# Kernel optimization log

Hardware: AMD Instinct MI355X
Metric: run time of the kernel (lower is better)

## Reference

```python
import jax, jax.numpy as jnp
import numpy as np

EPS = 1e-05

def setup_inputs() -> dict:
    key = jax.random.key(0)
    inputs = jax.random.normal(key, (32, 512, 768), dtype=jnp.float32)
    return {"inputs": inputs}

def reference(inputs) -> jnp.ndarray:
    # position weight: L2 norm per token, w[b,l] = sqrt(1e-5 + sum_d x^2)
    w = jnp.sqrt(EPS + jnp.sum(inputs * inputs, axis=-1))  # [B, L]
    # output[b,d,e] = sum_l w[b,l] * x[b,l,d] * x[b,l,e]
    # fused weighted Gram matrix; never materializes [B,L,D,D]
    return jnp.einsum('bld,ble->bde', inputs * w[..., None], inputs)
```

## Files before the change

kernel.cpp:

```cpp
#include <hip/hip_runtime.h>
#include <hip/hip_bf16.h>

#define BATCH 32
#define LL 512
#define DD 768
#define EPSC 1e-5f

typedef __attribute__((ext_vector_type(8))) short bf16x8;
typedef __attribute__((ext_vector_type(4))) float f32x4;

__global__ __launch_bounds__(256) void k_prep(const float* __restrict__ x,
                                              ushort* __restrict__ yt) {
    __shared__ float tile[64][65];
    __shared__ float svec[64];
    int lb = blockIdx.x;
    int b = blockIdx.y;
    int l0 = lb * 64;
    int t = threadIdx.x;

    {
        int r = t >> 2, q = t & 3;
        const float4* xr = (const float4*)(x + ((size_t)b * LL + l0 + r) * DD) + q * 48;
        float sum = 0.f;
#pragma unroll 8
        for (int i = 0; i < 48; i++) {
            float4 v = xr[i];
            sum += v.x * v.x + v.y * v.y + v.z * v.z + v.w * v.w;
        }
        sum += __shfl_xor(sum, 1, 64);
        sum += __shfl_xor(sum, 2, 64);
        if (q == 0) svec[r] = sqrtf(sqrtf(EPSC + sum));
    }
    __syncthreads();

    const float* xb = x + ((size_t)b * LL + l0) * DD;
    int f = t & 15, lr0 = t >> 4;
    int lc = t & 7, dl0 = t >> 3;
    for (int dt = 0; dt < 12; dt++) {
        int d0 = dt * 64;
#pragma unroll
        for (int r = 0; r < 4; r++) {
            int l = lr0 + r * 16;
            float4 v = *(const float4*)(xb + (size_t)l * DD + d0 + f * 4);
#pragma unroll
            for (int j = 0; j < 4; j++)
                tile[l][f * 4 + j] = ((const float*)&v)[j];
        }
        __syncthreads();
        ushort* yp = yt + ((size_t)b * DD + d0) * LL + l0;
#pragma unroll
        for (int it = 0; it < 2; it++) {
            int d = dl0 + it * 32;
            bf16x8 w;
#pragma unroll
            for (int j = 0; j < 8; j++) {
                int l = lc * 8 + j;
                float v = tile[l][d] * svec[l];
                __hip_bfloat16 h = __float2bfloat16(v);
                w[j] = *(short*)&h;
            }
            *(bf16x8*)(yp + (size_t)d * LL + lc * 8) = w;
        }
        __syncthreads();
    }
}

__global__ __launch_bounds__(256) void k_gemm(const ushort* __restrict__ yt,
                                              float* __restrict__ out) {
    __shared__ ushort At[2][128 * 64];
    __shared__ ushort Bt[2][128 * 64];
    int i = blockIdx.x;
    int xcd = i & 7, slot = i >> 3;
    int b = xcd + 8 * (slot / 21);
    int p = slot % 21;
    int t = p, tm = 0, rem = 6;
    while (t >= rem) { t -= rem; rem--; tm++; }
    int tn = tm + t;
    bool diag = (tm == tn);
    int m0 = tm * 128, n0 = tn * 128;
    int tid = threadIdx.x;
    int wave = tid >> 6, lane = tid & 63;
    int wr = wave >> 1, wc = wave & 1;
    const ushort* yb = yt + (size_t)b * DD * LL;

    f32x4 acc[4][4];
#pragma unroll
    for (int ii = 0; ii < 4; ii++)
#pragma unroll
        for (int j = 0; j < 4; j++) acc[ii][j] = (f32x4){0.f, 0.f, 0.f, 0.f};

    int sr[4], sc[4];
#pragma unroll
    for (int is = 0; is < 4; is++) {
        int s = is * 256 + tid;
        sr[is] = s >> 3;
        sc[is] = (s & 7) ^ (sr[is] & 7);
    }
    const ushort* gA[4];
    const ushort* gB[4];
#pragma unroll
    for (int is = 0; is < 4; is++) {
        gA[is] = yb + (size_t)(m0 + sr[is]) * LL + sc[is] * 8;
        gB[is] = yb + (size_t)(n0 + sr[is]) * LL + sc[is] * 8;
    }
    int ldsOff[4];
#pragma unroll
    for (int is = 0; is < 4; is++) ldsOff[is] = (is * 256 + wave * 64) * 8;

    int fr = lane & 15, ks4 = lane >> 4;

#define STAGE(buf, ks) do {                                                   \
        int k0_ = (ks) * 64;                                                  \
        _Pragma("unroll")                                                     \
        for (int is = 0; is < 4; is++)                                        \
            __builtin_amdgcn_global_load_lds(                                 \
                (const __attribute__((address_space(1))) void*)(gA[is] + k0_),\
                (__attribute__((address_space(3))) void*)(At[buf] + ldsOff[is]),\
                16, 0, 0);                                                    \
        if (!diag) {                                                          \
            _Pragma("unroll")                                                 \
            for (int is = 0; is < 4; is++)                                    \
                __builtin_amdgcn_global_load_lds(                             \
                    (const __attribute__((address_space(1))) void*)(gB[is] + k0_),\
                    (__attribute__((address_space(3))) void*)(Bt[buf] + ldsOff[is]),\
                    16, 0, 0);                                                \
        }                                                                     \
    } while (0)

    STAGE(0, 0);
    __syncthreads();
    for (int ks = 0; ks < 8; ks++) {
        int cur = ks & 1;
        if (ks < 7) STAGE(cur ^ 1, ks + 1);
        const ushort* Ab = At[cur];
        const ushort* Bb = diag ? At[cur] : Bt[cur];
        bf16x8 af[4][2], bf[4][2];
#pragma unroll
        for (int ii = 0; ii < 4; ii++) {
            int mr = wr * 64 + ii * 16 + fr;
            int nr = wc * 64 + ii * 16 + fr;
#pragma unroll
            for (int h = 0; h < 2; h++) {
                int slm = ((h * 4 + ks4) ^ (mr & 7)) * 8;
                int sln = ((h * 4 + ks4) ^ (nr & 7)) * 8;
                af[ii][h] = *(const bf16x8*)(Ab + mr * 64 + slm);
                bf[ii][h] = *(const bf16x8*)(Bb + nr * 64 + sln);
            }
        }
#pragma unroll
        for (int ii = 0; ii < 4; ii++)
#pragma unroll
            for (int j = 0; j < 4; j++)
#pragma unroll
                for (int h = 0; h < 2; h++)
                    acc[ii][j] = __builtin_amdgcn_mfma_f32_16x16x32_bf16(
                        af[ii][h], bf[j][h], acc[ii][j], 0, 0, 0);
        if (ks < 7) __syncthreads();
    }
#undef STAGE

    float* op = out + (size_t)b * DD * DD;
#pragma unroll
    for (int ii = 0; ii < 4; ii++) {
        int colb = m0 + wr * 64 + ii * 16 + ks4 * 4;
#pragma unroll
        for (int j = 0; j < 4; j++) {
            int row = n0 + wc * 64 + j * 16 + fr;
            float4 v = {acc[ii][j][0], acc[ii][j][1], acc[ii][j][2], acc[ii][j][3]};
            *(float4*)(op + (size_t)row * DD + colb) = v;
        }
    }
    if (!diag) {
#pragma unroll
        for (int ii = 0; ii < 4; ii++) {
            int mbase = m0 + wr * 64 + ii * 16 + ks4 * 4;
#pragma unroll
            for (int j = 0; j < 4; j++) {
                int n = n0 + wc * 64 + j * 16 + fr;
#pragma unroll
                for (int r = 0; r < 4; r++)
                    op[(size_t)(mbase + r) * DD + n] = acc[ii][j][r];
            }
        }
    }
}

extern "C" void kernel_launch(void* const* d_in, const int* in_sizes, int n_in,
                              void* d_out, int out_size, void* d_ws, size_t ws_size,
                              hipStream_t stream) {
    const float* x = (const float*)d_in[0];
    ushort* yt = (ushort*)d_ws;

    k_prep<<<dim3(LL / 64, BATCH), 256, 0, stream>>>(x, yt);
    k_gemm<<<dim3(21 * BATCH), 256, 0, stream>>>(yt, (float*)d_out);
}
```

Measured before the change: 133.0 us.

## Use single-wave 64x64 GEMM tiles with waitcnt-based double buffering

Replaces the 256-thread 128x128-tile Gram GEMM with a one-wave 64x64-tile kernel over 78 upper-triangle tiles per batch. This raises the block count from 672 to 2496. Because one wave owns its tile, it swaps __syncthreads for explicit s_waitcnt vmcnt on the async global->LDS loads. Diagonal tiles now load B redundantly. The aim is better occupancy and load balance and less barrier overhead, at the cost of lower data reuse per tile and more global traffic.

```diff
diff --git a/kernel.cpp b/kernel.cpp
--- a/kernel.cpp
+++ b/kernel.cpp
@@ -65,23 +65,32 @@
     }
 }
 
-__global__ __launch_bounds__(256) void k_gemm(const ushort* __restrict__ yt,
-                                              float* __restrict__ out) {
-    __shared__ ushort At[2][128 * 64];
-    __shared__ ushort Bt[2][128 * 64];
+__global__ __launch_bounds__(64) void k_gemm(const ushort* __restrict__ yt,
+                                             float* __restrict__ out) {
+    __shared__ ushort At[2][64 * 32];
+    __shared__ ushort Bt[2][64 * 32];
     int i = blockIdx.x;
     int xcd = i & 7, slot = i >> 3;
-    int b = xcd + 8 * (slot / 21);
-    int p = slot % 21;
-    int t = p, tm = 0, rem = 6;
+    int b = xcd + 8 * (slot / 78);
+    int p = slot % 78;
+    int t = p, tm = 0, rem = 12;
     while (t >= rem) { t -= rem; rem--; tm++; }
     int tn = tm + t;
     bool diag = (tm == tn);
-    int m0 = tm * 128, n0 = tn * 128;
-    int tid = threadIdx.x;
-    int wave = tid >> 6, lane = tid & 63;
-    int wr = wave >> 1, wc = wave & 1;
+    int m0 = tm * 64, n0 = tn * 64;
+    int lane = threadIdx.x;
+    int fr = lane & 15, ks4 = lane >> 4;
     const ushort* yb = yt + (size_t)b * DD * LL;
+
+    const ushort* gA[4];
+    int dBA = (n0 - m0) * LL;
+#pragma unroll
+    for (int is = 0; is < 4; is++) {
+        int s = is * 64 + lane;
+        int row = s >> 2;
+        int lc = (s & 3) ^ (row & 3);
+        gA[is] = yb + (size_t)(m0 + row) * LL + lc * 8;
+    }
 
     f32x4 acc[4][4];
 #pragma unroll
@@ -89,83 +98,58 @@
 #pragma unroll
         for (int j = 0; j < 4; j++) acc[ii][j] = (f32x4){0.f, 0.f, 0.f, 0.f};
 
-    int sr[4], sc[4];
-#pragma unroll
-    for (int is = 0; is < 4; is++) {
-        int s = is * 256 + tid;
-        sr[is] = s >> 3;
-        sc[is] = (s & 7) ^ (sr[is] & 7);
-    }
-    const ushort* gA[4];
-    const ushort* gB[4];
-#pragma unroll
-    for (int is = 0; is < 4; is++) {
-        gA[is] = yb + (size_t)(m0 + sr[is]) * LL + sc[is] * 8;
-        gB[is] = yb + (size_t)(n0 + sr[is]) * LL + sc[is] * 8;
-    }
-    int ldsOff[4];
-#pragma unroll
-    for (int is = 0; is < 4; is++) ldsOff[is] = (is * 256 + wave * 64) * 8;
-
-    int fr = lane & 15, ks4 = lane >> 4;
-
 #define STAGE(buf, ks) do {                                                   \
-        int k0_ = (ks) * 64;                                                  \
+        int k0_ = (ks) * 32;                                                  \
         _Pragma("unroll")                                                     \
         for (int is = 0; is < 4; is++)                                        \
             __builtin_amdgcn_global_load_lds(                                 \
                 (const __attribute__((address_space(1))) void*)(gA[is] + k0_),\
-                (__attribute__((address_space(3))) void*)(At[buf] + ldsOff[is]),\
+                (__attribute__((address_space(3))) void*)(At[buf] + is * 512),\
                 16, 0, 0);                                                    \
-        if (!diag) {                                                          \
-            _Pragma("unroll")                                                 \
-            for (int is = 0; is < 4; is++)                                    \
-                __builtin_amdgcn_global_load_lds(                             \
-                    (const __attribute__((address_space(1))) void*)(gB[is] + k0_),\
-                    (__attribute__((address_space(3))) void*)(Bt[buf] + ldsOff[is]),\
-                    16, 0, 0);                                                \
-        }                                                                     \
+        _Pragma("unroll")                                                     \
+        for (int is = 0; is < 4; is++)                                        \
+            __builtin_amdgcn_global_load_lds(                                 \
+                (const __attribute__((address_space(1))) void*)(gA[is] + dBA + k0_),\
+                (__attribute__((address_space(3))) void*)(Bt[buf] + is * 512),\
+                16, 0, 0);                                                    \
     } while (0)
 
     STAGE(0, 0);
-    __syncthreads();
-    for (int ks = 0; ks < 8; ks++) {
+    for (int ks = 0; ks < 16; ks++) {
         int cur = ks & 1;
-        if (ks < 7) STAGE(cur ^ 1, ks + 1);
+        if (ks < 15) {
+            STAGE(cur ^ 1, ks + 1);
+            asm volatile("s_waitcnt vmcnt(8)" ::: "memory");
+        } else {
+            asm volatile("s_waitcnt vmcnt(0)" ::: "memory");
+        }
+        __builtin_amdgcn_sched_barrier(0);
         const ushort* Ab = At[cur];
-        const ushort* Bb = diag ? At[cur] : Bt[cur];
-        bf16x8 af[4][2], bf[4][2];
+        const ushort* Bb = Bt[cur];
+        bf16x8 af[4], bg[4];
 #pragma unroll
         for (int ii = 0; ii < 4; ii++) {
-            int mr = wr * 64 + ii * 16 + fr;
-            int nr = wc * 64 + ii * 16 + fr;
-#pragma unroll
-            for (int h = 0; h < 2; h++) {
-                int slm = ((h * 4 + ks4) ^ (mr & 7)) * 8;
-                int sln = ((h * 4 + ks4) ^ (nr & 7)) * 8;
-                af[ii][h] = *(const bf16x8*)(Ab + mr * 64 + slm);
-                bf[ii][h] = *(const bf16x8*)(Bb + nr * 64 + sln);
-            }
+            int mr = ii * 16 + fr;
+            int ca = ks4 ^ (mr & 3);
+            af[ii] = *(const bf16x8*)(Ab + mr * 32 + ca * 8);
+            bg[ii] = *(const bf16x8*)(Bb + mr * 32 + ca * 8);
         }
 #pragma unroll
         for (int ii = 0; ii < 4; ii++)
 #pragma unroll
             for (int j = 0; j < 4; j++)
-#pragma unroll
-                for (int h = 0; h < 2; h++)
-                    acc[ii][j] = __builtin_amdgcn_mfma_f32_16x16x32_bf16(
-                        af[ii][h], bf[j][h], acc[ii][j], 0, 0, 0);
-        if (ks < 7) __syncthreads();
+                acc[ii][j] = __builtin_amdgcn_mfma_f32_16x16x32_bf16(
+                    af[ii], bg[j], acc[ii][j], 0, 0, 0);
     }
 #undef STAGE
 
     float* op = out + (size_t)b * DD * DD;
 #pragma unroll
     for (int ii = 0; ii < 4; ii++) {
-        int colb = m0 + wr * 64 + ii * 16 + ks4 * 4;
+        int colb = m0 + ii * 16 + ks4 * 4;
 #pragma unroll
         for (int j = 0; j < 4; j++) {
-            int row = n0 + wc * 64 + j * 16 + fr;
+            int row = n0 + j * 16 + fr;
             float4 v = {acc[ii][j][0], acc[ii][j][1], acc[ii][j][2], acc[ii][j][3]};
             *(float4*)(op + (size_t)row * DD + colb) = v;
         }
@@ -173,10 +157,10 @@
     if (!diag) {
 #pragma unroll
         for (int ii = 0; ii < 4; ii++) {
-            int mbase = m0 + wr * 64 + ii * 16 + ks4 * 4;
+            int mbase = m0 + ii * 16 + ks4 * 4;
 #pragma unroll
             for (int j = 0; j < 4; j++) {
-                int n = n0 + wc * 64 + j * 16 + fr;
+                int n = n0 + j * 16 + fr;
 #pragma unroll
                 for (int r = 0; r < 4; r++)
                     op[(size_t)(mbase + r) * DD + n] = acc[ii][j][r];
@@ -192,5 +176,5 @@
     ushort* yt = (ushort*)d_ws;
 
     k_prep<<<dim3(LL / 64, BATCH), 256, 0, stream>>>(x, yt);
-    k_gemm<<<dim3(21 * BATCH), 256, 0, stream>>>(yt, (float*)d_out);
+    k_gemm<<<dim3(78 * BATCH), 64, 0, stream>>>(yt, (float*)d_out);
 }
```

After: 140.0 us. +5.3%, slower.
